# Optimization experiments

Hardware: AMD Instinct MI355X
Metric: run time of the kernel (lower is better)

## Reference

```python
import jax, jax.numpy as jnp
import numpy as np

B, T, D_MODEL, N_HEADS = 2, 2048, 1024, 16
HEAD_DIM = D_MODEL // N_HEADS
GN_EPS = 1e-5


def decay_gammas(n_heads):
    # gamma_h = 1 - 2^(-5 - h*(8/n_heads))
    h = jnp.arange(n_heads, dtype=jnp.float32)
    return 1.0 - jnp.power(2.0, -5.0 - h * (8.0 / n_heads))


def setup_inputs() -> dict:
    key = jax.random.key(0)
    ks = jax.random.split(key, 7)
    w_scale = 0.02
    return {
        "x": jax.random.normal(ks[0], (B, T, D_MODEL), dtype=jnp.float32),
        "Wq": jax.random.normal(ks[1], (D_MODEL, D_MODEL), dtype=jnp.float32) * w_scale,
        "Wk": jax.random.normal(ks[2], (D_MODEL, D_MODEL), dtype=jnp.float32) * w_scale,
        "Wv": jax.random.normal(ks[3], (D_MODEL, D_MODEL), dtype=jnp.float32) * w_scale,
        "Wo": jax.random.normal(ks[4], (D_MODEL, D_MODEL), dtype=jnp.float32) * w_scale,
        "gn_w": jnp.ones((D_MODEL,), dtype=jnp.float32),
        "gn_b": jnp.zeros((D_MODEL,), dtype=jnp.float32),
    }


def reference(x, Wq, Wk, Wv, Wo, gn_w, gn_b):
    Bx, Tx, C = x.shape
    H, D = N_HEADS, C // N_HEADS
    gammas = decay_gammas(H)  # (H,)

    def split_heads(y):
        return y.reshape(Bx, Tx, H, D).transpose(0, 2, 1, 3)  # (B,H,T,D)

    # torch Linear: y = x @ W.T
    Q = split_heads(x @ Wq.T)
    K = split_heads(x @ Wk.T)
    V = split_heads(x @ Wv.T)

    # causal decay mask D[h,i,j] = gamma_h^(i-j) if i>=j else 0
    idx = jnp.arange(Tx, dtype=jnp.float32)
    diff = idx[:, None] - idx[None, :]  # (T,T)
    mask = jnp.where(diff >= 0,
                     gammas[:, None, None] ** jnp.maximum(diff, 0.0),
                     0.0)  # (H,T,T)

    scores = jnp.einsum("bhtd,bhsd->bhts", Q, K) / jnp.sqrt(jnp.float32(D))
    scores = scores * mask[None]  # (B,H,T,T)
    out = jnp.einsum("bhts,bhsd->bhtd", scores, V)  # (B,H,T,D)
    y = out.transpose(0, 2, 1, 3).reshape(Bx, Tx, C)  # merge heads

    # GroupNorm(n_heads, d_model) applied on (B, C, T): normalizes over
    # (head_dim, T) per group per batch element.
    z = y.transpose(0, 2, 1).reshape(Bx, H, D, Tx)
    mu = z.mean(axis=(2, 3), keepdims=True)
    var = z.var(axis=(2, 3), keepdims=True)
    zn = (z - mu) * jax.lax.rsqrt(var + GN_EPS)
    zn = zn * gn_w.reshape(1, H, D, 1) + gn_b.reshape(1, H, D, 1)
    y = zn.reshape(Bx, C, Tx).transpose(0, 2, 1)  # (B,T,C)

    return y @ Wo.T
```

## Files before the change

### kernel.cpp

```cpp
#include <hip/hip_runtime.h>
#include <hip/hip_bf16.h>

typedef __attribute__((ext_vector_type(8))) short short8;
typedef __attribute__((ext_vector_type(4))) float float4v;
typedef __attribute__((ext_vector_type(16))) float float16v;
typedef unsigned short u16;
typedef unsigned long long ull;

#define KD 1024

__device__ __forceinline__ u16 f2b(float f) {
    __hip_bfloat16 h = __float2bfloat16(f);
    return __builtin_bit_cast(u16, h);
}
__device__ __forceinline__ float b2f(u16 u) {
    unsigned x = ((unsigned)u) << 16;
    return __builtin_bit_cast(float, x);
}
__device__ __forceinline__ float lg_gamma(int h) {
    float gamma = 1.0f - exp2f(-5.0f - 0.5f * (float)h);
    return log2f(gamma);
}

__device__ __forceinline__ void async_cp16(const u16* g, u16* l) {
    __builtin_amdgcn_global_load_lds(
        (const __attribute__((address_space(1))) void*)g,
        (__attribute__((address_space(3))) void*)l,
        16, 0, 0);
}

__global__ __launch_bounds__(256)
void cvt_all(const float* __restrict__ x, const float* __restrict__ wq,
             const float* __restrict__ wk, const float* __restrict__ wv,
             const float* __restrict__ wo,
             u16* __restrict__ xb, u16* __restrict__ wqkvb, u16* __restrict__ wob)
{
    int bid = blockIdx.x;
    if (bid < 4096) {
        long i = (long)bid * 1024 + threadIdx.x * 4;
        float4 v = *(const float4*)(x + i);
        ushort4 u;
        u.x = f2b(v.x); u.y = f2b(v.y); u.z = f2b(v.z); u.w = f2b(v.w);
        *(ushort4*)(xb + i) = u;
    } else {
        int wbid = bid - 4096;
        int mtx = wbid >> 10;
        int n = wbid & 1023;
        const float* src = (mtx == 0) ? wq : (mtx == 1) ? wk : (mtx == 2) ? wv : wo;
        u16* dst = (mtx == 3) ? wob : (wqkvb + (size_t)mtx * 1048576);
        float sc = (mtx == 0) ? 0.125f : 1.0f;
        int k0 = threadIdx.x * 4;
        float4 v = *(const float4*)(src + (size_t)n * 1024 + k0);
        int panel = n >> 5, row = n & 31, kg = k0 >> 4, kh = (k0 >> 3) & 1, off = k0 & 7;
        size_t o = (size_t)panel * 32768 + (size_t)kg * 512 + kh * 256 + row * 8 + off;
        ushort4 u;
        u.x = f2b(v.x * sc); u.y = f2b(v.y * sc); u.z = f2b(v.z * sc); u.w = f2b(v.w * sc);
        *(ushort4*)(dst + o) = u;
    }
}

template<int MODE>
__global__ __launch_bounds__(256)
void gemm_nt(const u16* __restrict__ A, const u16* __restrict__ Bpk,
             u16* __restrict__ oQ, u16* __restrict__ oK,
             u16* __restrict__ oKt, u16* __restrict__ oVt,
             float* __restrict__ of)
{
    constexpr int TM = (MODE == 0) ? 128 : 64;
    constexpr int MI = (MODE == 0) ? 2 : 1;
    __shared__ __attribute__((aligned(16))) u16 Sh[(MODE == 0) ? 16384 : 4096];
    u16* As = Sh;
    const int tid = threadIdx.x;
    const int lane = tid & 63;
    const int wv = tid >> 6;
    const int wm = wv >> 1, wn = wv & 1;
    const int row32 = lane & 31, khalf = lane >> 5;
    const int lrow = lane >> 3, lseg = lane & 7;
    const int lin = blockIdx.x + gridDim.x * blockIdx.y;
    const int xcd = lin & 7, idx = lin >> 3;
    int m_tile, n_tile;
    if (MODE == 0) { m_tile = (idx & 3) + 4 * xcd; n_tile = idx >> 2; }
    else           { m_tile = (idx & 7) + 8 * xcd; n_tile = idx >> 3; }
    const int m0 = m_tile * TM, n0 = n_tile * 128;

    float16v acc[MI][2];
#pragma unroll
    for (int i = 0; i < MI; i++)
#pragma unroll
        for (int j = 0; j < 2; j++)
#pragma unroll
            for (int r = 0; r < 16; r++) acc[i][j][r] = 0.f;

    const int scol = (lseg ^ lrow) << 3;
    const u16* bp = Bpk + (size_t)((n0 >> 5) + wn * 2) * 32768 + (size_t)lane * 8;

    for (int kt = 0; kt < KD; kt += 64) {
        __syncthreads();
#pragma unroll
        for (int i = 0; i < TM / 32; i++) {
            int r = wv * (TM / 4) + i * 8;
            async_cp16(A + (size_t)(m0 + r + lrow) * KD + kt + scol, &As[r * 64]);
        }
        short8 bgl[4][2];
#pragma unroll
        for (int ks = 0; ks < 4; ks++)
#pragma unroll
            for (int j = 0; j < 2; j++)
                bgl[ks][j] = *(const short8*)(bp + (size_t)j * 32768 + ((kt >> 4) + ks) * 512);
        __syncthreads();
#pragma unroll
        for (int ks = 0; ks < 4; ks++) {
            short8 af[MI];
#pragma unroll
            for (int i = 0; i < MI; i++) {
                int row = wm * (MI * 32) + i * 32 + row32;
                af[i] = *(const short8*)(&As[row * 64 + (((ks * 2 + khalf) ^ (row & 7)) << 3)]);
            }
#pragma unroll
            for (int i = 0; i < MI; i++)
#pragma unroll
                for (int j = 0; j < 2; j++)
                    acc[i][j] = __builtin_amdgcn_mfma_f32_32x32x16_bf16(af[i], bgl[ks][j], acc[i][j], 0, 0, 0);
        }
    }

    if (MODE == 0) {
        const int wsel = n0 >> 10;
        if (wsel <= 1) {
            u16* dst = (wsel == 0) ? oQ : oK;
#pragma unroll
            for (int i = 0; i < 2; i++)
#pragma unroll
                for (int j = 0; j < 2; j++) {
                    int gn = n0 + wn * 64 + j * 32 + row32;
                    int dd = gn & 63, hh = (gn >> 6) & 15;
#pragma unroll
                    for (int reg = 0; reg < 16; reg++) {
                        int m = m0 + wm * 64 + i * 32 + (reg & 3) + 8 * (reg >> 2) + 4 * khalf;
                        int b = m >> 11, t = m & 2047;
                        dst[(size_t)(b * 16 + hh) * 131072 + t * 64 + dd] = f2b(acc[i][j][reg]);
                    }
                }
        }
        if (wsel >= 1) {
            __syncthreads();
            u16* Tl = Sh + wv * 4096;
#pragma unroll
            for (int i = 0; i < 2; i++)
#pragma unroll
                for (int j = 0; j < 2; j++) {
                    int n_loc = j * 32 + row32;
#pragma unroll
                    for (int g = 0; g < 4; g++) {
                        int m4 = i * 32 + 8 * g + 4 * khalf;
                        ull pk = (ull)f2b(acc[i][j][4 * g]) | ((ull)f2b(acc[i][j][4 * g + 1]) << 16) |
                                 ((ull)f2b(acc[i][j][4 * g + 2]) << 32) | ((ull)f2b(acc[i][j][4 * g + 3]) << 48);
                        *(ull*)(&Tl[n_loc * 64 + (((m4 >> 3) ^ (n_loc & 7)) << 3) + (m4 & 7)]) = pk;
                    }
                }
            __syncthreads();
            int gnb = n0 + wn * 64;
            int hh = (gnb >> 6) & 15;
            int mb = m0 + wm * 64;
            int bh = (mb >> 11) * 16 + hh;
            int t0 = mb & 2047;
            u16* dstT = (wsel == 1) ? oKt : oVt;
            int rr = lane >> 3, ss = lane & 7;
#pragma unroll
            for (int g = 0; g < 8; g++) {
                int row = 8 * g + rr;
                short8 v = *(const short8*)(&Tl[row * 64 + ((ss ^ rr) << 3)]);
                *(short8*)(&dstT[(size_t)bh * 131072 + (size_t)row * 2048 + t0 + ss * 8]) = v;
            }
        }
    } else {
        int gn0 = n0 + wn * 64 + row32;
#pragma unroll
        for (int g = 0; g < 4; g++)
#pragma unroll
            for (int rr = 0; rr < 4; rr++) {
                int reg = 4 * g + rr;
                int m = m0 + wm * 32 + 8 * g + 4 * khalf + rr;
                of[(size_t)m * 1024 + gn0] = acc[0][0][reg];
                of[(size_t)m * 1024 + gn0 + 32] = acc[0][1][reg];
            }
    }
}

__global__ __launch_bounds__(256)
void chunk_state(const u16* __restrict__ Kt, const u16* __restrict__ Vt,
                 u16* __restrict__ U)
{
    const int c = blockIdx.x, bh = blockIdx.y, h = bh & 15;
    const int tid = threadIdx.x, lane = tid & 63, w = tid >> 6;
    const int row16 = lane & 15, quad = lane >> 4;
    const float lg = lg_gamma(h);
    const size_t base = (size_t)bh * 131072;

    float4v acc[4];
    float4v zero4 = {0.f, 0.f, 0.f, 0.f};
#pragma unroll
    for (int tn = 0; tn < 4; tn++) acc[tn] = zero4;

#pragma unroll
    for (int kb = 0; kb < 2; kb++) {
        short8 a = *(const short8*)(Vt + base + (size_t)(16 * w + row16) * 2048 + c * 64 + kb * 32 + quad * 8);
        short8 as;
        int e0 = 63 - (kb * 32 + quad * 8);
#pragma unroll
        for (int jj = 0; jj < 8; jj++) {
            float v = b2f((u16)a[jj]) * exp2f(lg * (float)(e0 - jj));
            as[jj] = (short)f2b(v);
        }
#pragma unroll
        for (int tn = 0; tn < 4; tn++) {
            short8 bfr = *(const short8*)(Kt + base + (size_t)(16 * tn + row16) * 2048 + c * 64 + kb * 32 + quad * 8);
            acc[tn] = __builtin_amdgcn_mfma_f32_16x16x32_bf16(as, bfr, acc[tn], 0, 0, 0);
        }
    }
    u16* up = U + ((size_t)bh * 32 + c) * 4096;
#pragma unroll
    for (int tn = 0; tn < 4; tn++)
#pragma unroll
        for (int r = 0; r < 4; r++)
            up[(16 * w + quad * 4 + r) * 64 + 16 * tn + row16] = f2b(acc[tn][r]);
}

__global__ __launch_bounds__(256)
void state_scan(const u16* __restrict__ U, u16* __restrict__ St)
{
    const int bh = blockIdx.y;
    const int e = blockIdx.x * 256 + threadIdx.x;
    const float g64 = exp2f(lg_gamma(bh & 15) * 64.0f);
    float s = 0.f;
    St[(size_t)bh * 131072 + e] = 0;
    for (int c = 1; c < 32; c++) {
        s = g64 * s + b2f(U[((size_t)bh * 32 + (c - 1)) * 4096 + e]);
        St[((size_t)bh * 32 + c) * 4096 + e] = f2b(s);
    }
}

__global__ __launch_bounds__(256)
void retention_chunk(const u16* __restrict__ Q, const u16* __restrict__ Kb,
                     const u16* __restrict__ Vt, const u16* __restrict__ St,
                     float* __restrict__ Y, float* __restrict__ stats)
{
    __shared__ __attribute__((aligned(16))) u16 Pl[4][16 * 72];
    __shared__ float red[8];
    const int c = blockIdx.x, bh = blockIdx.y, h = bh & 15;
    const int tid = threadIdx.x, lane = tid & 63, w = tid >> 6;
    const int row16 = lane & 15, quad = lane >> 4;
    const float lg = lg_gamma(h);
    const size_t base = (size_t)bh * 131072;
    float4v zero4 = {0.f, 0.f, 0.f, 0.f};

    short8 qf[2];
#pragma unroll
    for (int kb = 0; kb < 2; kb++)
        qf[kb] = *(const short8*)(Q + base + (size_t)(c * 64 + 16 * w + row16) * 64 + kb * 32 + quad * 8);

    float4v accp[4];
#pragma unroll
    for (int tn = 0; tn < 4; tn++) accp[tn] = zero4;
#pragma unroll
    for (int tn = 0; tn < 4; tn++)
#pragma unroll
        for (int kb = 0; kb < 2; kb++) {
            short8 kf = *(const short8*)(Kb + base + (size_t)(c * 64 + 16 * tn + row16) * 64 + kb * 32 + quad * 8);
            accp[tn] = __builtin_amdgcn_mfma_f32_16x16x32_bf16(qf[kb], kf, accp[tn], 0, 0, 0);
        }
#pragma unroll
    for (int tn = 0; tn < 4; tn++)
#pragma unroll
        for (int r = 0; r < 4; r++) {
            int a_loc = 16 * w + quad * 4 + r;
            int b_loc = 16 * tn + row16;
            int d = a_loc - b_loc;
            float v = (d >= 0) ? accp[tn][r] * exp2f(lg * (float)d) : 0.f;
            Pl[w][(quad * 4 + r) * 72 + b_loc] = f2b(v);
        }
    __syncthreads();

    short8 pf[2];
#pragma unroll
    for (int kb = 0; kb < 2; kb++)
        pf[kb] = *(const short8*)(&Pl[w][row16 * 72 + kb * 32 + quad * 8]);

    float4v acco[4], acci[4];
#pragma unroll
    for (int tn = 0; tn < 4; tn++) { acco[tn] = zero4; acci[tn] = zero4; }
#pragma unroll
    for (int tn = 0; tn < 4; tn++)
#pragma unroll
        for (int kb = 0; kb < 2; kb++) {
            short8 vf = *(const short8*)(Vt + base + (size_t)(16 * tn + row16) * 2048 + c * 64 + kb * 32 + quad * 8);
            acco[tn] = __builtin_amdgcn_mfma_f32_16x16x32_bf16(pf[kb], vf, acco[tn], 0, 0, 0);
            short8 sf = *(const short8*)(St + ((size_t)bh * 32 + c) * 4096 + (16 * tn + row16) * 64 + kb * 32 + quad * 8);
            acci[tn] = __builtin_amdgcn_mfma_f32_16x16x32_bf16(qf[kb], sf, acci[tn], 0, 0, 0);
        }

    float s = 0.f, s2 = 0.f;
#pragma unroll
    for (int tn = 0; tn < 4; tn++)
#pragma unroll
        for (int r = 0; r < 4; r++) {
            int a_loc = 16 * w + quad * 4 + r;
            float gi = exp2f(lg * (float)(a_loc + 1));
            int t = c * 64 + a_loc, d2 = 16 * tn + row16;
            float yv = acco[tn][r] + gi * acci[tn][r];
            Y[(size_t)bh * 131072 + t * 64 + d2] = yv;
            s += yv;
            s2 += yv * yv;
        }
#pragma unroll
    for (int off = 32; off; off >>= 1) {
        s += __shfl_down(s, off, 64);
        s2 += __shfl_down(s2, off, 64);
    }
    if (lane == 0) { red[w] = s; red[4 + w] = s2; }
    __syncthreads();
    if (tid == 0) {
        atomicAdd(&stats[2 * bh], red[0] + red[1] + red[2] + red[3]);
        atomicAdd(&stats[2 * bh + 1], red[4] + red[5] + red[6] + red[7]);
    }
}

__global__ __launch_bounds__(256)
void gn_apply(const float* __restrict__ Y, const float* __restrict__ stats,
              const float* __restrict__ gnw, const float* __restrict__ gnb,
              u16* __restrict__ Z)
{
    int i4 = (blockIdx.x * 256 + threadIdx.x) * 4;
    int b = i4 >> 21, t = (i4 >> 10) & 2047, cc = i4 & 1023;
    int hh = cc >> 6, dd = cc & 63, bh = b * 16 + hh;
    float4 v = *(const float4*)(Y + (size_t)bh * 131072 + t * 64 + dd);
    float S = stats[2 * bh], S2 = stats[2 * bh + 1];
    float mu = S * (1.0f / 131072.f);
    float var = S2 * (1.0f / 131072.f) - mu * mu;
    float rsg = rsqrtf(var + 1e-5f);
    float4 wv = *(const float4*)(gnw + cc);
    float4 bv = *(const float4*)(gnb + cc);
    ushort4 o;
    o.x = f2b((v.x - mu) * rsg * wv.x + bv.x);
    o.y = f2b((v.y - mu) * rsg * wv.y + bv.y);
    o.z = f2b((v.z - mu) * rsg * wv.z + bv.z);
    o.w = f2b((v.w - mu) * rsg * wv.w + bv.w);
    *(ushort4*)(Z + i4) = o;
}

extern "C" void kernel_launch(void* const* d_in, const int* in_sizes, int n_in,
                              void* d_out, int out_size, void* d_ws, size_t ws_size,
                              hipStream_t stream) {
    const float* x   = (const float*)d_in[0];
    const float* Wq  = (const float*)d_in[1];
    const float* Wk  = (const float*)d_in[2];
    const float* Wv  = (const float*)d_in[3];
    const float* Wo  = (const float*)d_in[4];
    const float* gnw = (const float*)d_in[5];
    const float* gnb = (const float*)d_in[6];
    float* out = (float*)d_out;
    char* ws = (char*)d_ws;

    u16*  xb    = (u16*)(ws + 0);
    u16*  wqkvb = (u16*)(ws + 8388608);
    u16*  wob   = (u16*)(ws + 14680064);
    u16*  Qs    = (u16*)(ws + 16777216);
    u16*  Kb    = (u16*)(ws + 25165824);
    u16*  Kt    = (u16*)(ws + 33554432);
    u16*  Vt    = (u16*)(ws + 41943040);
    u16*  U     = (u16*)(ws + 50331648);
    u16*  St    = (u16*)(ws + 67108864);
    float* Y    = (float*)(ws + 75497472);
    u16*  Zb    = (u16*)(ws + 92274688);
    float* stats= (float*)(ws + 100663296);

    hipMemsetAsync(stats, 0, 64 * sizeof(float), stream);

    cvt_all<<<8192, 256, 0, stream>>>(x, Wq, Wk, Wv, Wo, xb, wqkvb, wob);

    gemm_nt<0><<<dim3(24, 32), 256, 0, stream>>>(xb, wqkvb, Qs, Kb, Kt, Vt, nullptr);

    chunk_state<<<dim3(32, 32), 256, 0, stream>>>(Kt, Vt, U);
    state_scan<<<dim3(16, 32), 256, 0, stream>>>(U, St);
    retention_chunk<<<dim3(32, 32), 256, 0, stream>>>(Qs, Kb, Vt, St, Y, stats);

    gn_apply<<<4096, 256, 0, stream>>>(Y, stats, gnw, gnb, Zb);

    gemm_nt<1><<<dim3(8, 64), 256, 0, stream>>>(Zb, wob, nullptr, nullptr, nullptr, nullptr, out);
}
```

Before: 185.1 us.

## Vectorize weight packing, remap GEMM tiles per XCD, store retention output as bf16

The weight-conversion kernel now has each thread write 16 contiguous packed elements with 16-byte stores, using fewer blocks, instead of scattered 8-byte stores. The GEMM block-to-tile mapping changes so that each XCD handles its own set of N columns, which is meant to improve L2 reuse of weight panels. The retention output Y is stored as bf16 rather than fp32, halving the write and read traffic between retention_chunk and gn_apply. The bf16 rounding of Y before group normalization costs some accuracy, while the statistics are still accumulated in fp32.

After: 185.6 us. No clear change (+0.3%).

```diff
diff --git a/kernel.cpp b/kernel.cpp
--- a/kernel.cpp
+++ b/kernel.cpp
@@ -44,18 +44,26 @@
         *(ushort4*)(xb + i) = u;
     } else {
         int wbid = bid - 4096;
-        int mtx = wbid >> 10;
-        int n = wbid & 1023;
+        int mtx = wbid >> 8;
+        int panel = (wbid & 255) >> 3, ks = wbid & 7;
         const float* src = (mtx == 0) ? wq : (mtx == 1) ? wk : (mtx == 2) ? wv : wo;
         u16* dst = (mtx == 3) ? wob : (wqkvb + (size_t)mtx * 1048576);
         float sc = (mtx == 0) ? 0.125f : 1.0f;
-        int k0 = threadIdx.x * 4;
-        float4 v = *(const float4*)(src + (size_t)n * 1024 + k0);
-        int panel = n >> 5, row = n & 31, kg = k0 >> 4, kh = (k0 >> 3) & 1, off = k0 & 7;
-        size_t o = (size_t)panel * 32768 + (size_t)kg * 512 + kh * 256 + row * 8 + off;
-        ushort4 u;
-        u.x = f2b(v.x * sc); u.y = f2b(v.y * sc); u.z = f2b(v.z * sc); u.w = f2b(v.w * sc);
-        *(ushort4*)(dst + o) = u;
+        int idx = threadIdx.x * 16;
+        int kg = idx >> 9, kh = (idx >> 8) & 1, r0 = (idx & 255) >> 3;
+        int k0 = ks * 128 + kg * 16 + kh * 8;
+        int row = panel * 32 + r0;
+        const float* s0 = src + (size_t)row * 1024 + k0;
+        float4 a0 = ((const float4*)s0)[0], a1 = ((const float4*)s0)[1];
+        float4 b0 = ((const float4*)(s0 + 1024))[0], b1 = ((const float4*)(s0 + 1024))[1];
+        short8 o0, o1;
+        o0[0]=f2b(a0.x*sc); o0[1]=f2b(a0.y*sc); o0[2]=f2b(a0.z*sc); o0[3]=f2b(a0.w*sc);
+        o0[4]=f2b(a1.x*sc); o0[5]=f2b(a1.y*sc); o0[6]=f2b(a1.z*sc); o0[7]=f2b(a1.w*sc);
+        o1[0]=f2b(b0.x*sc); o1[1]=f2b(b0.y*sc); o1[2]=f2b(b0.z*sc); o1[3]=f2b(b0.w*sc);
+        o1[4]=f2b(b1.x*sc); o1[5]=f2b(b1.y*sc); o1[6]=f2b(b1.z*sc); o1[7]=f2b(b1.w*sc);
+        u16* d = dst + (size_t)panel * 32768 + ks * 4096 + idx;
+        *(short8*)d = o0;
+        *(short8*)(d + 8) = o1;
     }
 }
 
@@ -76,11 +84,11 @@
     const int wm = wv >> 1, wn = wv & 1;
     const int row32 = lane & 31, khalf = lane >> 5;
     const int lrow = lane >> 3, lseg = lane & 7;
-    const int lin = blockIdx.x + gridDim.x * blockIdx.y;
+    const int lin = blockIdx.x;
     const int xcd = lin & 7, idx = lin >> 3;
     int m_tile, n_tile;
-    if (MODE == 0) { m_tile = (idx & 3) + 4 * xcd; n_tile = idx >> 2; }
-    else           { m_tile = (idx & 7) + 8 * xcd; n_tile = idx >> 3; }
+    if (MODE == 0) { m_tile = idx & 31; n_tile = xcd * 3 + (idx >> 5); }
+    else           { m_tile = idx;      n_tile = xcd; }
     const int m0 = m_tile * TM, n0 = n_tile * 128;
 
     float16v acc[MI][2];
@@ -243,7 +251,7 @@
 __global__ __launch_bounds__(256)
 void retention_chunk(const u16* __restrict__ Q, const u16* __restrict__ Kb,
                      const u16* __restrict__ Vt, const u16* __restrict__ St,
-                     float* __restrict__ Y, float* __restrict__ stats)
+                     u16* __restrict__ Y, float* __restrict__ stats)
 {
     __shared__ __attribute__((aligned(16))) u16 Pl[4][16 * 72];
     __shared__ float red[8];
@@ -308,7 +316,7 @@
             float gi = exp2f(lg * (float)(a_loc + 1));
             int t = c * 64 + a_loc, d2 = 16 * tn + row16;
             float yv = acco[tn][r] + gi * acci[tn][r];
-            Y[(size_t)bh * 131072 + t * 64 + d2] = yv;
+            Y[(size_t)bh * 131072 + t * 64 + d2] = f2b(yv);
             s += yv;
             s2 += yv * yv;
         }
@@ -326,14 +334,14 @@
 }
 
 __global__ __launch_bounds__(256)
-void gn_apply(const float* __restrict__ Y, const float* __restrict__ stats,
+void gn_apply(const u16* __restrict__ Y, const float* __restrict__ stats,
               const float* __restrict__ gnw, const float* __restrict__ gnb,
               u16* __restrict__ Z)
 {
     int i4 = (blockIdx.x * 256 + threadIdx.x) * 4;
     int b = i4 >> 21, t = (i4 >> 10) & 2047, cc = i4 & 1023;
     int hh = cc >> 6, dd = cc & 63, bh = b * 16 + hh;
-    float4 v = *(const float4*)(Y + (size_t)bh * 131072 + t * 64 + dd);
+    ushort4 yv4 = *(const ushort4*)(Y + (size_t)bh * 131072 + t * 64 + dd);
     float S = stats[2 * bh], S2 = stats[2 * bh + 1];
     float mu = S * (1.0f / 131072.f);
     float var = S2 * (1.0f / 131072.f) - mu * mu;
@@ -341,10 +349,10 @@
     float4 wv = *(const float4*)(gnw + cc);
     float4 bv = *(const float4*)(gnb + cc);
     ushort4 o;
-    o.x = f2b((v.x - mu) * rsg * wv.x + bv.x);
-    o.y = f2b((v.y - mu) * rsg * wv.y + bv.y);
-    o.z = f2b((v.z - mu) * rsg * wv.z + bv.z);
-    o.w = f2b((v.w - mu) * rsg * wv.w + bv.w);
+    o.x = f2b((b2f(yv4.x) - mu) * rsg * wv.x + bv.x);
+    o.y = f2b((b2f(yv4.y) - mu) * rsg * wv.y + bv.y);
+    o.z = f2b((b2f(yv4.z) - mu) * rsg * wv.z + bv.z);
+    o.w = f2b((b2f(yv4.w) - mu) * rsg * wv.w + bv.w);
     *(ushort4*)(Z + i4) = o;
 }
 
@@ -370,15 +378,15 @@
     u16*  Vt    = (u16*)(ws + 41943040);
     u16*  U     = (u16*)(ws + 50331648);
     u16*  St    = (u16*)(ws + 67108864);
-    float* Y    = (float*)(ws + 75497472);
+    u16*  Y     = (u16*)(ws + 75497472);
     u16*  Zb    = (u16*)(ws + 92274688);
     float* stats= (float*)(ws + 100663296);
 
     hipMemsetAsync(stats, 0, 64 * sizeof(float), stream);
 
-    cvt_all<<<8192, 256, 0, stream>>>(x, Wq, Wk, Wv, Wo, xb, wqkvb, wob);
-
-    gemm_nt<0><<<dim3(24, 32), 256, 0, stream>>>(xb, wqkvb, Qs, Kb, Kt, Vt, nullptr);
+    cvt_all<<<5120, 256, 0, stream>>>(x, Wq, Wk, Wv, Wo, xb, wqkvb, wob);
+
+    gemm_nt<0><<<768, 256, 0, stream>>>(xb, wqkvb, Qs, Kb, Kt, Vt, nullptr);
 
     chunk_state<<<dim3(32, 32), 256, 0, stream>>>(Kt, Vt, U);
     state_scan<<<dim3(16, 32), 256, 0, stream>>>(U, St);
@@ -386,5 +394,5 @@
 
     gn_apply<<<4096, 256, 0, stream>>>(Y, stats, gnw, gnb, Zb);
 
-    gemm_nt<1><<<dim3(8, 64), 256, 0, stream>>>(Zb, wob, nullptr, nullptr, nullptr, nullptr, out);
-}
+    gemm_nt<1><<<512, 256, 0, stream>>>(Zb, wob, nullptr, nullptr, nullptr, nullptr, out);
+}
```
